# Kernel tuning notes

Measured on AMD Instinct MI355X. Metric: run time of the kernel, lower is better.

Reference implementation:

```python
import jax, jax.numpy as jnp
import numpy as np

N_NODES = 50000
N_EDGES = 1_600_000
DIMS = [512, 256, 128]


def _edge_softmax(vals, rows, n):
    # sparse softmax over dim=1 (per source row), only over stored edges
    m = jax.ops.segment_max(vals, rows, num_segments=n)
    e = jnp.exp(vals - m[rows])
    s = jax.ops.segment_sum(e, rows, num_segments=n)
    return e / s[rows]


def _spmm(att, rows, cols, H, n):
    # (sparse C) @ H : gather source cols, scale by edge weight, scatter-add to rows
    return jax.ops.segment_sum(att[:, None] * H[cols], rows, num_segments=n)


def setup_inputs() -> dict:
    key = jax.random.key(0)
    ks = jax.random.split(key, 12)
    X = jax.random.normal(ks[0], (N_NODES, DIMS[0]), dtype=jnp.float32)
    edge_row = jax.random.randint(ks[1], (N_EDGES,), 0, N_NODES, dtype=jnp.int32)
    edge_col = jax.random.randint(ks[2], (N_EDGES,), 0, N_NODES, dtype=jnp.int32)
    A_vals = jnp.ones((N_EDGES,), dtype=jnp.float32)
    def lin(k, dout, din):
        lim = 1.0 / np.sqrt(din)
        return jax.random.uniform(k, (dout, din), jnp.float32, -lim, lim)
    W0 = lin(ks[3], DIMS[1], DIMS[0])
    b0 = jax.random.uniform(ks[4], (DIMS[1],), jnp.float32, -1/np.sqrt(DIMS[0]), 1/np.sqrt(DIMS[0]))
    W1 = lin(ks[5], DIMS[2], DIMS[1])
    b1 = jax.random.uniform(ks[6], (DIMS[2],), jnp.float32, -1/np.sqrt(DIMS[1]), 1/np.sqrt(DIMS[1]))
    v00 = jax.random.normal(ks[7], (DIMS[1],), dtype=jnp.float32)
    v01 = jax.random.normal(ks[8], (DIMS[1],), dtype=jnp.float32)
    v10 = jax.random.normal(ks[9], (DIMS[2],), dtype=jnp.float32)
    v11 = jax.random.normal(ks[10], (DIMS[2],), dtype=jnp.float32)
    return {"X": X, "edge_row": edge_row, "edge_col": edge_col, "A_vals": A_vals,
            "W0": W0, "b0": b0, "W1": W1, "b1": b1,
            "v00": v00, "v01": v01, "v10": v10, "v11": v11}


def reference(X, edge_row, edge_col, A_vals, W0, b0, W1, b1, v00, v01, v10, v11):
    n = X.shape[0]
    layers = [((W0, b0), (v00, v01)), ((W1, b1), (v10, v11))]
    H = X
    atts = []
    # encoder
    for (W, b), (va, vb) in layers:
        M = H @ W.T + b                               # [N, d_out]
        # attention logits are computed under no_grad in the original
        f1 = M @ va                                   # [N]
        f2 = M @ vb
        logits = jax.lax.stop_gradient(A_vals * (f1[edge_row] + f2[edge_col]))
        att = _edge_softmax(jax.nn.sigmoid(logits), edge_row, n)
        H = _spmm(att, edge_row, edge_col, M, n)
        atts.append(att)
    final_H = H
    # decoder (tied weights, reverse order, reuse encoder attention)
    for ((W, _), _), att in zip(reversed(layers), reversed(atts)):
        H = H @ W                                     # F.linear(H, W.t()) == H @ W
        H = _spmm(att, edge_row, edge_col, H, n)
    return H, final_H
```

## Files before the change

### kernel.cpp

```cpp
#include <hip/hip_runtime.h>
#include <cstdint>
#include <cstddef>

typedef __attribute__((ext_vector_type(8))) short bf16x8;
typedef __attribute__((ext_vector_type(4))) float f32x4;

__device__ __forceinline__ ushort f2b(float f) {
    union { float f; uint32_t u; } v; v.f = f;
    uint32_t r = (v.u + 0x7fffu + ((v.u >> 16) & 1u)) >> 16;
    return (ushort)r;
}
__device__ __forceinline__ float b2f(ushort b) {
    union { uint32_t u; float f; } v; v.u = ((uint32_t)b) << 16;
    return v.f;
}

__device__ __forceinline__ void gll16(const void* g, void* l) {
    __builtin_amdgcn_global_load_lds((const __attribute__((address_space(1))) void*)g,
                                     (__attribute__((address_space(3))) void*)l, 16, 0, 0);
}

__global__ __launch_bounds__(256) void hist_kernel(const int* __restrict__ rows,
                                                   int* __restrict__ bhist, int E, int nb) {
    __shared__ int h[512];
    for (int i = threadIdx.x; i < nb; i += 256) h[i] = 0;
    __syncthreads();
    int stride = gridDim.x * blockDim.x;
    for (int e = blockIdx.x * blockDim.x + threadIdx.x; e < E; e += stride)
        atomicAdd(&h[rows[e] >> 7], 1);
    __syncthreads();
    for (int i = threadIdx.x; i < nb; i += 256)
        if (h[i]) atomicAdd(&bhist[i], h[i]);
}

__global__ __launch_bounds__(512) void scan512(const int* __restrict__ bhist,
                                               int* __restrict__ boff, int* __restrict__ gcur,
                                               int* __restrict__ rp, int nb, int E, int N) {
    __shared__ int sm[512];
    int v = ((int)threadIdx.x < nb) ? bhist[threadIdx.x] : 0;
    sm[threadIdx.x] = v;
    __syncthreads();
    for (int off = 1; off < 512; off <<= 1) {
        int t = ((int)threadIdx.x >= off) ? sm[threadIdx.x - off] : 0;
        __syncthreads();
        sm[threadIdx.x] += t;
        __syncthreads();
    }
    if ((int)threadIdx.x < nb) {
        int e0 = sm[threadIdx.x] - v;
        boff[threadIdx.x] = e0;
        gcur[threadIdx.x] = e0;
    }
    if (threadIdx.x == 0) { boff[nb] = E; rp[N] = E; }
}

__global__ __launch_bounds__(256) void binpass(const int* __restrict__ rows,
                                               const int* __restrict__ cols,
                                               const float* __restrict__ avals,
                                               int* __restrict__ gcur,
                                               uint2* __restrict__ tmp, int E, int nb) {
    __shared__ int hist[512];
    __shared__ int base[512];
    int e0 = blockIdx.x * 4096;
    int nE = min(4096, E - e0);
    for (int i = threadIdx.x; i < nb; i += 256) hist[i] = 0;
    __syncthreads();
    for (int i = threadIdx.x; i < nE; i += 256)
        atomicAdd(&hist[rows[e0 + i] >> 7], 1);
    __syncthreads();
    for (int i = threadIdx.x; i < nb; i += 256) {
        int c = hist[i];
        if (c) base[i] = atomicAdd(&gcur[i], c);
        hist[i] = 0;
    }
    __syncthreads();
    for (int i = threadIdx.x; i < nE; i += 256) {
        int r = rows[e0 + i];
        int b = r >> 7;
        int loc = atomicAdd(&hist[b], 1);
        uint2 t;
        t.x = ((uint32_t)r << 16) | (uint32_t)cols[e0 + i];
        t.y = __float_as_uint(avals[e0 + i]);
        tmp[base[b] + loc] = t;
    }
}

__global__ __launch_bounds__(256) void bucketpass(const uint2* __restrict__ tmp,
                                                  const int* __restrict__ boff,
                                                  int* __restrict__ rp,
                                                  int* __restrict__ col_s,
                                                  float* __restrict__ a_s, int N) {
    __shared__ int cnt[128];
    __shared__ int pre[128];
    int b = blockIdx.x;
    int r0 = b << 7;
    int nr = min(128, N - r0);
    int t0 = boff[b], t1 = boff[b + 1];
    if ((int)threadIdx.x < 128) cnt[threadIdx.x] = 0;
    __syncthreads();
    for (int i = t0 + (int)threadIdx.x; i < t1; i += 256)
        atomicAdd(&cnt[(tmp[i].x >> 16) - r0], 1);
    __syncthreads();
    if ((int)threadIdx.x < 128) pre[threadIdx.x] = cnt[threadIdx.x];
    __syncthreads();
    for (int off = 1; off < 128; off <<= 1) {
        int t = ((int)threadIdx.x >= off && (int)threadIdx.x < 128) ? pre[threadIdx.x - off] : 0;
        __syncthreads();
        if ((int)threadIdx.x < 128) pre[threadIdx.x] += t;
        __syncthreads();
    }
    if ((int)threadIdx.x < nr) {
        int ex = pre[threadIdx.x] - cnt[threadIdx.x];
        rp[r0 + threadIdx.x] = t0 + ex;
        cnt[threadIdx.x] = t0 + ex;
    }
    __syncthreads();
    for (int i = t0 + (int)threadIdx.x; i < t1; i += 256) {
        uint2 t = tmp[i];
        int lr = (int)(t.x >> 16) - r0;
        int pos = atomicAdd(&cnt[lr], 1);
        col_s[pos] = (int)(t.x & 0xffffu);
        a_s[pos] = __uint_as_float(t.y);
    }
}

__global__ __launch_bounds__(256) void wprep(const float* __restrict__ W0,
                                             const float* __restrict__ W1,
                                             const float* __restrict__ b0,
                                             const float* __restrict__ v00,
                                             const float* __restrict__ v01,
                                             float* __restrict__ u0,
                                             float* __restrict__ u1,
                                             float* __restrict__ bp,
                                             float* __restrict__ cc) {
    if (blockIdx.x == 0) {
        int c = threadIdx.x;
        for (int rep = 0; rep < 2; ++rep, c += 256) {
            float s0 = 0.f, s1 = 0.f;
            for (int r = 0; r < 256; ++r) {
                float w = W0[(size_t)r * 512 + c];
                s0 += w * v00[r];
                s1 += w * v01[r];
            }
            u0[c] = s0;
            u1[c] = s1;
        }
    } else {
        int i = threadIdx.x;
        if (i < 128) {
            float s = 0.f;
            for (int k = 0; k < 256; ++k) s += W1[(size_t)i * 256 + k] * b0[k];
            bp[i] = s;
        } else if (i == 128) {
            float s = 0.f;
            for (int k = 0; k < 256; ++k) s += b0[k] * v00[k];
            cc[0] = s;
        } else if (i == 129) {
            float s = 0.f;
            for (int k = 0; k < 256; ++k) s += b0[k] * v01[k];
            cc[1] = s;
        }
    }
}

__global__ __launch_bounds__(256) void convert_fx(const float* __restrict__ X,
                                                  const float* __restrict__ u0,
                                                  const float* __restrict__ u1,
                                                  const float* __restrict__ cc,
                                                  ushort* __restrict__ Xh,
                                                  float* __restrict__ f1,
                                                  float* __restrict__ f2, int N) {
    int w = threadIdx.x >> 6;
    int l = threadIdx.x & 63;
    const float4* U0 = (const float4*)u0;
    const float4* U1 = (const float4*)u1;
    float4 ua = U0[l * 2], ub = U0[l * 2 + 1];
    float4 va = U1[l * 2], vb = U1[l * 2 + 1];
    float c0 = cc[0], c1 = cc[1];
#pragma unroll
    for (int rr = 0; rr < 2; ++rr) {
        int row = blockIdx.x * 8 + w * 2 + rr;
        if (row >= N) return;
        const float4* Xr = (const float4*)(X + (size_t)row * 512);
        float4 x0 = Xr[l * 2], x1 = Xr[l * 2 + 1];
        ushort4 h0, h1;
        h0.x = f2b(x0.x); h0.y = f2b(x0.y); h0.z = f2b(x0.z); h0.w = f2b(x0.w);
        h1.x = f2b(x1.x); h1.y = f2b(x1.y); h1.z = f2b(x1.z); h1.w = f2b(x1.w);
        ushort4* Xo = (ushort4*)(Xh + (size_t)row * 512);
        Xo[l * 2] = h0;
        Xo[l * 2 + 1] = h1;
        float s1 = x0.x * ua.x + x0.y * ua.y + x0.z * ua.z + x0.w * ua.w
                 + x1.x * ub.x + x1.y * ub.y + x1.z * ub.z + x1.w * ub.w;
        float s2 = x0.x * va.x + x0.y * va.y + x0.z * va.z + x0.w * va.w
                 + x1.x * vb.x + x1.y * vb.y + x1.z * vb.z + x1.w * vb.w;
#pragma unroll
        for (int off = 32; off > 0; off >>= 1) {
            s1 += __shfl_xor(s1, off);
            s2 += __shfl_xor(s2, off);
        }
        if (l == 0) { f1[row] = s1 + c0; f2[row] = s2 + c1; }
    }
}

__global__ __launch_bounds__(256) void prep_weights(const float* __restrict__ W0,
                                                    const float* __restrict__ W1,
                                                    ushort* __restrict__ W1h,
                                                    ushort* __restrict__ Wt0h) {
    int i = blockIdx.x * 256 + threadIdx.x;
    float4 v = ((const float4*)W0)[i];
    ushort4 o;
    o.x = f2b(v.x); o.y = f2b(v.y); o.z = f2b(v.z); o.w = f2b(v.w);
    int r = (i * 4) >> 9;
    int c = (i * 4) & 511;
    Wt0h[(size_t)(c + 0) * 256 + r] = o.x;
    Wt0h[(size_t)(c + 1) * 256 + r] = o.y;
    Wt0h[(size_t)(c + 2) * 256 + r] = o.z;
    Wt0h[(size_t)(c + 3) * 256 + r] = o.w;
    if (i < 8192) {
        float4 w = ((const float4*)W1)[i];
        ushort4 p;
        p.x = f2b(w.x); p.y = f2b(w.y); p.z = f2b(w.z); p.w = f2b(w.w);
        ((ushort4*)W1h)[i] = p;
    }
}

__global__ __launch_bounds__(256) void gemm_bf16(const ushort* __restrict__ A,
                                                 const ushort* __restrict__ B,
                                                 const float* __restrict__ bias,
                                                 float* __restrict__ Cf,
                                                 ushort* __restrict__ Ch,
                                                 ushort* __restrict__ ChT,
                                                 int M, int K, int Dout) {
    __shared__ ushort As[128 * 64];
    __shared__ ushort Bs[128 * 64];
    int bm = blockIdx.y * 128, bn = blockIdx.x * 128;
    int tid = threadIdx.x;
    int w = tid >> 6, l = tid & 63;
    int wm = (w & 1) * 64, wn = (w >> 1) * 64;
    int lm = l & 15, quad = l >> 4;
    int wslot = tid & 192;

    f32x4 acc[4][4] = {};

    for (int k0 = 0; k0 < K; k0 += 64) {
#pragma unroll
        for (int it = 0; it < 4; ++it) {
            int slot = it * 256 + tid;
            int row = slot >> 3;
            int qg = ((slot & 7) ^ (row & 7)) * 8;
            int ga = bm + row; if (ga > M - 1) ga = M - 1;
            gll16(A + (size_t)ga * K + k0 + qg, As + (size_t)(it * 256 + wslot) * 8);
            gll16(B + (size_t)(bn + row) * K + k0 + qg, Bs + (size_t)(it * 256 + wslot) * 8);
        }
        __syncthreads();
#pragma unroll
        for (int ks = 0; ks < 2; ++ks) {
            bf16x8 af[4], bfr[4];
#pragma unroll
            for (int i = 0; i < 4; ++i) {
                int r = wm + i * 16 + lm;
                af[i] = *(const bf16x8*)&As[r * 64 + (((ks * 4 + quad) ^ (r & 7)) * 8)];
            }
#pragma unroll
            for (int j = 0; j < 4; ++j) {
                int r = wn + j * 16 + lm;
                bfr[j] = *(const bf16x8*)&Bs[r * 64 + (((ks * 4 + quad) ^ (r & 7)) * 8)];
            }
#pragma unroll
            for (int i = 0; i < 4; ++i)
#pragma unroll
                for (int j = 0; j < 4; ++j)
                    acc[i][j] = __builtin_amdgcn_mfma_f32_16x16x32_bf16(af[i], bfr[j], acc[i][j], 0, 0, 0);
        }
        __syncthreads();
    }

    float bv[4] = {0.f, 0.f, 0.f, 0.f};
    if (bias) {
#pragma unroll
        for (int j = 0; j < 4; ++j) bv[j] = bias[bn + wn + j * 16 + lm];
    }
#pragma unroll
    for (int i = 0; i < 4; ++i) {
#pragma unroll
        for (int r = 0; r < 4; ++r) {
            int row = bm + wm + i * 16 + quad * 4 + r;
            if (row < M) {
#pragma unroll
                for (int j = 0; j < 4; ++j) {
                    int col = bn + wn + j * 16 + lm;
                    float v = acc[i][j][r] + bv[j];
                    if (Cf) Cf[(size_t)row * Dout + col] = v;
                    if (Ch) Ch[(size_t)row * Dout + col] = f2b(v);
                    if (ChT) ChT[(size_t)col * M + row] = f2b(v);
                }
            }
        }
    }
}

__global__ __launch_bounds__(256) void att2_kernel(const int* __restrict__ rp,
                                                   const int* __restrict__ col_s,
                                                   const float* __restrict__ a_s,
                                                   const float* __restrict__ f1,
                                                   const float* __restrict__ f2,
                                                   float* __restrict__ att,
                                                   float* __restrict__ rs, int N) {
    int r = blockIdx.x * 4 + (threadIdx.x >> 6);
    if (r >= N) return;
    int lane = threadIdx.x & 63;
    int beg = rp[r], end = rp[r + 1];
    float fr = f1[r];
    float s = 0.f;
    for (int j = beg + lane; j < end; j += 64) {
        float x = a_s[j] * (fr + f2[col_s[j]]);
        float v = 1.f / (1.f + __expf(-x));
        float e = __expf(v);
        att[j] = e;
        s += e;
    }
#pragma unroll
    for (int off = 32; off > 0; off >>= 1) s += __shfl_xor(s, off);
    if (lane == 0) rs[r] = (end > beg) ? 1.f / s : 0.f;
}

__global__ __launch_bounds__(256) void spmm128(const int* __restrict__ rp,
                                               const int* __restrict__ col_s,
                                               const float* __restrict__ att,
                                               const float* __restrict__ rs,
                                               const ushort* __restrict__ H,
                                               const float* __restrict__ bias,
                                               const float* __restrict__ va,
                                               const float* __restrict__ vb,
                                               float* __restrict__ f1,
                                               float* __restrict__ f2,
                                               ushort* __restrict__ Oh,
                                               float* __restrict__ Of, int N) {
    int r = blockIdx.x * 16 + (threadIdx.x >> 4);
    if (r >= N) return;
    int lane = threadIdx.x & 15;
    int beg = rp[r], end = rp[r + 1];
    float acc[8] = {0.f, 0.f, 0.f, 0.f, 0.f, 0.f, 0.f, 0.f};
    const uint4* H4 = (const uint4*)H;
#define FMA8(h, wgt) { \
        acc[0] += (wgt) * b2f((ushort)((h).x & 0xffffu)); \
        acc[1] += (wgt) * b2f((ushort)((h).x >> 16)); \
        acc[2] += (wgt) * b2f((ushort)((h).y & 0xffffu)); \
        acc[3] += (wgt) * b2f((ushort)((h).y >> 16)); \
        acc[4] += (wgt) * b2f((ushort)((h).z & 0xffffu)); \
        acc[5] += (wgt) * b2f((ushort)((h).z >> 16)); \
        acc[6] += (wgt) * b2f((ushort)((h).w & 0xffffu)); \
        acc[7] += (wgt) * b2f((ushort)((h).w >> 16)); }
    int j = beg;
    for (; j + 4 <= end; j += 4) {
        int c0 = col_s[j], c1 = col_s[j + 1], c2 = col_s[j + 2], c3 = col_s[j + 3];
        float w0 = att[j], w1 = att[j + 1], w2 = att[j + 2], w3 = att[j + 3];
        uint4 h0 = H4[(size_t)c0 * 16 + lane];
        uint4 h1 = H4[(size_t)c1 * 16 + lane];
        uint4 h2 = H4[(size_t)c2 * 16 + lane];
        uint4 h3 = H4[(size_t)c3 * 16 + lane];
        FMA8(h0, w0) FMA8(h1, w1) FMA8(h2, w2) FMA8(h3, w3)
    }
    for (; j < end; ++j) {
        uint4 h = H4[(size_t)col_s[j] * 16 + lane];
        float w0 = att[j];
        FMA8(h, w0)
    }
#undef FMA8
    float rsv = rs[r];
#pragma unroll
    for (int k = 0; k < 8; ++k) acc[k] *= rsv;
    if (bias) {
        const float4* b4 = (const float4*)(bias + lane * 8);
        float4 ba = b4[0], bb = b4[1];
        acc[0] += ba.x; acc[1] += ba.y; acc[2] += ba.z; acc[3] += ba.w;
        acc[4] += bb.x; acc[5] += bb.y; acc[6] += bb.z; acc[7] += bb.w;
    }
    if (va) {
        const float4* a4 = (const float4*)(va + lane * 8);
        const float4* c4 = (const float4*)(vb + lane * 8);
        float4 va0 = a4[0], va1 = a4[1], vb0 = c4[0], vb1 = c4[1];
        float p1 = acc[0] * va0.x + acc[1] * va0.y + acc[2] * va0.z + acc[3] * va0.w
                 + acc[4] * va1.x + acc[5] * va1.y + acc[6] * va1.z + acc[7] * va1.w;
        float p2 = acc[0] * vb0.x + acc[1] * vb0.y + acc[2] * vb0.z + acc[3] * vb0.w
                 + acc[4] * vb1.x + acc[5] * vb1.y + acc[6] * vb1.z + acc[7] * vb1.w;
#pragma unroll
        for (int off = 8; off > 0; off >>= 1) {
            p1 += __shfl_xor(p1, off);
            p2 += __shfl_xor(p2, off);
        }
        if (lane == 0) { f1[r] = p1; f2[r] = p2; }
    }
    if (Oh) {
        uint4 o;
        o.x = (uint32_t)f2b(acc[0]) | ((uint32_t)f2b(acc[1]) << 16);
        o.y = (uint32_t)f2b(acc[2]) | ((uint32_t)f2b(acc[3]) << 16);
        o.z = (uint32_t)f2b(acc[4]) | ((uint32_t)f2b(acc[5]) << 16);
        o.w = (uint32_t)f2b(acc[6]) | ((uint32_t)f2b(acc[7]) << 16);
        ((uint4*)Oh)[(size_t)r * 16 + lane] = o;
    }
    if (Of) {
        float4* O4 = (float4*)Of;
        O4[(size_t)r * 32 + lane * 2]     = make_float4(acc[0], acc[1], acc[2], acc[3]);
        O4[(size_t)r * 32 + lane * 2 + 1] = make_float4(acc[4], acc[5], acc[6], acc[7]);
    }
}

extern "C" void kernel_launch(void* const* d_in, const int* in_sizes, int n_in,
                              void* d_out, int out_size, void* d_ws, size_t ws_size,
                              hipStream_t stream) {
    const float* X    = (const float*)d_in[0];
    const int*   erow = (const int*)d_in[1];
    const int*   ecol = (const int*)d_in[2];
    const float* aval = (const float*)d_in[3];
    const float* W0   = (const float*)d_in[4];
    const float* b0   = (const float*)d_in[5];
    const float* W1   = (const float*)d_in[6];
    const float* b1   = (const float*)d_in[7];
    const float* v00  = (const float*)d_in[8];
    const float* v01  = (const float*)d_in[9];
    const float* v10  = (const float*)d_in[10];
    const float* v11  = (const float*)d_in[11];

    const int D0 = 512, D1 = 256, D2 = 128;
    const int N = in_sizes[0] / D0;
    const int E = in_sizes[1];
    const int NB = (N + 127) / 128;
    float* out = (float*)d_out;

    char* ws = (char*)d_ws;
    size_t off = 0;
    auto alloc = [&](size_t bytes) {
        char* p = ws + off;
        off += (bytes + 255) & ~(size_t)255;
        return p;
    };
    ushort* Xh   = (ushort*)alloc((size_t)N * D0 * 2);
    ushort* Ph   = (ushort*)alloc((size_t)N * D2 * 2);
    ushort* M1h  = (ushort*)alloc((size_t)N * D2 * 2);
    ushort* H2h  = (ushort*)alloc((size_t)N * D2 * 2);
    ushort* S0h  = (ushort*)alloc((size_t)N * D2 * 2);
    ushort* W1h  = (ushort*)alloc((size_t)D2 * D1 * 2);
    ushort* Wt0h = (ushort*)alloc((size_t)D0 * D1 * 2);
    ushort* Wph  = (ushort*)alloc((size_t)D2 * D0 * 2);
    ushort* WfTh = (ushort*)alloc((size_t)D0 * D2 * 2);
    float* att0  = (float*)alloc((size_t)E * 4);
    float* att1  = (float*)alloc((size_t)E * 4);
    float* a_s   = (float*)alloc((size_t)E * 4);
    float* f1    = (float*)alloc((size_t)N * 4);
    float* f2    = (float*)alloc((size_t)N * 4);
    float* rs0   = (float*)alloc((size_t)N * 4);
    float* rs1   = (float*)alloc((size_t)N * 4);
    float* u0    = (float*)alloc(512 * 4);
    float* u1    = (float*)alloc(512 * 4);
    float* bp    = (float*)alloc(128 * 4);
    float* cc    = (float*)alloc(2 * 4);
    int* rp      = (int*)alloc(((size_t)N + 1) * 4);
    int* col_s   = (int*)alloc((size_t)E * 4);
    uint2* tmp   = (uint2*)alloc((size_t)E * 8);
    int* bhist   = (int*)alloc(512 * 4);
    int* boff    = (int*)alloc(513 * 4);
    int* gcur    = (int*)alloc(512 * 4);

    hipMemsetAsync(bhist, 0, 512 * sizeof(int), stream);
    hist_kernel<<<256, 256, 0, stream>>>(erow, bhist, E, NB);
    scan512<<<1, 512, 0, stream>>>(bhist, boff, gcur, rp, NB, E, N);
    binpass<<<(E + 4095) / 4096, 256, 0, stream>>>(erow, ecol, aval, gcur, tmp, E, NB);
    bucketpass<<<NB, 256, 0, stream>>>(tmp, boff, rp, col_s, a_s, N);

    wprep<<<2, 256, 0, stream>>>(W0, W1, b0, v00, v01, u0, u1, bp, cc);
    prep_weights<<<128, 256, 0, stream>>>(W0, W1, W1h, Wt0h);

    convert_fx<<<(N + 7) / 8, 256, 0, stream>>>(X, u0, u1, cc, Xh, f1, f2, N);

    gemm_bf16<<<dim3(4, 1), 256, 0, stream>>>(W1h, Wt0h, nullptr, nullptr, Wph, WfTh,
                                              D2, D1, D0);

    const int gy = (N + 127) / 128;
    const int agrid = (N + 3) / 4;
    const int sgrid = (N + 15) / 16;

    att2_kernel<<<agrid, 256, 0, stream>>>(rp, col_s, a_s, f1, f2, att0, rs0, N);
    gemm_bf16<<<dim3(1, gy), 256, 0, stream>>>(Xh, Wph, bp, nullptr, Ph, nullptr,
                                               N, D0, D2);
    spmm128<<<sgrid, 256, 0, stream>>>(rp, col_s, att0, rs0, Ph, b1, v10, v11, f1, f2,
                                       M1h, nullptr, N);
    att2_kernel<<<agrid, 256, 0, stream>>>(rp, col_s, a_s, f1, f2, att1, rs1, N);
    spmm128<<<sgrid, 256, 0, stream>>>(rp, col_s, att1, rs1, M1h, nullptr,
                                       nullptr, nullptr, nullptr, nullptr,
                                       H2h, out + (size_t)N * D0, N);

    spmm128<<<sgrid, 256, 0, stream>>>(rp, col_s, att1, rs1, H2h, nullptr,
                                       nullptr, nullptr, nullptr, nullptr,
                                       Ph, nullptr, N);
    spmm128<<<sgrid, 256, 0, stream>>>(rp, col_s, att0, rs0, Ph, nullptr,
                                       nullptr, nullptr, nullptr, nullptr,
                                       S0h, nullptr, N);
    gemm_bf16<<<dim3(D0 / 128, gy), 256, 0, stream>>>(S0h, WfTh, nullptr, out, nullptr,
                                                      nullptr, N, D2, D0);
}
```

Baseline: 661.4 us.

## Fuse X bf16 conversion and attention logits into the first GEMM

Replaces the separate convert_fx pass, which wrote a bf16 copy of X and computed f1/f2, with a GEMM that reads fp32 X directly, converts it to bf16 into LDS, and accumulates the f1/f2 dot products along the way. This removes one full write and re-read of the 50000x512 X copy. The weight-prep kernels are merged into one launch with a parallelised u0/u1 reduction, and the SpMM gather loop gains an 8-wide unroll for more loads in flight. In exchange, the GEMM now stages A through registers instead of async global-to-LDS loads, which may expose more latency.

Result: faster. 612.6 us (-7.4%).

```diff
diff --git a/kernel.cpp b/kernel.cpp
--- a/kernel.cpp
+++ b/kernel.cpp
@@ -13,6 +13,12 @@
 __device__ __forceinline__ float b2f(ushort b) {
     union { uint32_t u; float f; } v; v.u = ((uint32_t)b) << 16;
     return v.f;
+}
+__device__ __forceinline__ uint32_t pack2(float a, float b) {
+    return (uint32_t)f2b(a) | ((uint32_t)f2b(b) << 16);
+}
+__device__ __forceinline__ float dot4(float4 a, float4 b) {
+    return a.x * b.x + a.y * b.y + a.z * b.z + a.w * b.w;
 }
 
 __device__ __forceinline__ void gll16(const void* g, void* l) {
@@ -124,29 +130,59 @@
     }
 }
 
-__global__ __launch_bounds__(256) void wprep(const float* __restrict__ W0,
-                                             const float* __restrict__ W1,
-                                             const float* __restrict__ b0,
-                                             const float* __restrict__ v00,
-                                             const float* __restrict__ v01,
-                                             float* __restrict__ u0,
-                                             float* __restrict__ u1,
-                                             float* __restrict__ bp,
-                                             float* __restrict__ cc) {
-    if (blockIdx.x == 0) {
-        int c = threadIdx.x;
-        for (int rep = 0; rep < 2; ++rep, c += 256) {
-            float s0 = 0.f, s1 = 0.f;
-            for (int r = 0; r < 256; ++r) {
-                float w = W0[(size_t)r * 512 + c];
-                s0 += w * v00[r];
-                s1 += w * v01[r];
-            }
-            u0[c] = s0;
-            u1[c] = s1;
+__global__ __launch_bounds__(256) void prep_all(const float* __restrict__ W0,
+                                                const float* __restrict__ W1,
+                                                const float* __restrict__ b0,
+                                                const float* __restrict__ v00,
+                                                const float* __restrict__ v01,
+                                                ushort* __restrict__ W1h,
+                                                ushort* __restrict__ Wt0h,
+                                                float* __restrict__ u0,
+                                                float* __restrict__ u1,
+                                                float* __restrict__ bp,
+                                                float* __restrict__ cc) {
+    __shared__ float su0[256];
+    __shared__ float su1[256];
+    int bid = blockIdx.x;
+    int tid = threadIdx.x;
+    if (bid < 128) {
+        int i = bid * 256 + tid;
+        float4 v = ((const float4*)W0)[i];
+        ushort4 o;
+        o.x = f2b(v.x); o.y = f2b(v.y); o.z = f2b(v.z); o.w = f2b(v.w);
+        int r = (i * 4) >> 9;
+        int c = (i * 4) & 511;
+        Wt0h[(size_t)(c + 0) * 256 + r] = o.x;
+        Wt0h[(size_t)(c + 1) * 256 + r] = o.y;
+        Wt0h[(size_t)(c + 2) * 256 + r] = o.z;
+        Wt0h[(size_t)(c + 3) * 256 + r] = o.w;
+        if (i < 8192) {
+            float4 w = ((const float4*)W1)[i];
+            ushort4 p;
+            p.x = f2b(w.x); p.y = f2b(w.y); p.z = f2b(w.z); p.w = f2b(w.w);
+            ((ushort4*)W1h)[i] = p;
+        }
+    } else if (bid < 144) {
+        int ci = tid & 31;
+        int rl = tid >> 5;
+        int c = (bid - 128) * 32 + ci;
+        float s0 = 0.f, s1 = 0.f;
+        for (int r = rl; r < 256; r += 8) {
+            float w = W0[(size_t)r * 512 + c];
+            s0 += w * v00[r];
+            s1 += w * v01[r];
+        }
+        su0[tid] = s0;
+        su1[tid] = s1;
+        __syncthreads();
+        if (tid < 32) {
+            float a = 0.f, b = 0.f;
+            for (int g = 0; g < 8; ++g) { a += su0[g * 32 + tid]; b += su1[g * 32 + tid]; }
+            u0[c] = a;
+            u1[c] = b;
         }
     } else {
-        int i = threadIdx.x;
+        int i = tid;
         if (i < 128) {
             float s = 0.f;
             for (int k = 0; k < 256; ++k) s += W1[(size_t)i * 256 + k] * b0[k];
@@ -160,67 +196,6 @@
             for (int k = 0; k < 256; ++k) s += b0[k] * v01[k];
             cc[1] = s;
         }
-    }
-}
-
-__global__ __launch_bounds__(256) void convert_fx(const float* __restrict__ X,
-                                                  const float* __restrict__ u0,
-                                                  const float* __restrict__ u1,
-                                                  const float* __restrict__ cc,
-                                                  ushort* __restrict__ Xh,
-                                                  float* __restrict__ f1,
-                                                  float* __restrict__ f2, int N) {
-    int w = threadIdx.x >> 6;
-    int l = threadIdx.x & 63;
-    const float4* U0 = (const float4*)u0;
-    const float4* U1 = (const float4*)u1;
-    float4 ua = U0[l * 2], ub = U0[l * 2 + 1];
-    float4 va = U1[l * 2], vb = U1[l * 2 + 1];
-    float c0 = cc[0], c1 = cc[1];
-#pragma unroll
-    for (int rr = 0; rr < 2; ++rr) {
-        int row = blockIdx.x * 8 + w * 2 + rr;
-        if (row >= N) return;
-        const float4* Xr = (const float4*)(X + (size_t)row * 512);
-        float4 x0 = Xr[l * 2], x1 = Xr[l * 2 + 1];
-        ushort4 h0, h1;
-        h0.x = f2b(x0.x); h0.y = f2b(x0.y); h0.z = f2b(x0.z); h0.w = f2b(x0.w);
-        h1.x = f2b(x1.x); h1.y = f2b(x1.y); h1.z = f2b(x1.z); h1.w = f2b(x1.w);
-        ushort4* Xo = (ushort4*)(Xh + (size_t)row * 512);
-        Xo[l * 2] = h0;
-        Xo[l * 2 + 1] = h1;
-        float s1 = x0.x * ua.x + x0.y * ua.y + x0.z * ua.z + x0.w * ua.w
-                 + x1.x * ub.x + x1.y * ub.y + x1.z * ub.z + x1.w * ub.w;
-        float s2 = x0.x * va.x + x0.y * va.y + x0.z * va.z + x0.w * va.w
-                 + x1.x * vb.x + x1.y * vb.y + x1.z * vb.z + x1.w * vb.w;
-#pragma unroll
-        for (int off = 32; off > 0; off >>= 1) {
-            s1 += __shfl_xor(s1, off);
-            s2 += __shfl_xor(s2, off);
-        }
-        if (l == 0) { f1[row] = s1 + c0; f2[row] = s2 + c1; }
-    }
-}
-
-__global__ __launch_bounds__(256) void prep_weights(const float* __restrict__ W0,
-                                                    const float* __restrict__ W1,
-                                                    ushort* __restrict__ W1h,
-                                                    ushort* __restrict__ Wt0h) {
-    int i = blockIdx.x * 256 + threadIdx.x;
-    float4 v = ((const float4*)W0)[i];
-    ushort4 o;
-    o.x = f2b(v.x); o.y = f2b(v.y); o.z = f2b(v.z); o.w = f2b(v.w);
-    int r = (i * 4) >> 9;
-    int c = (i * 4) & 511;
-    Wt0h[(size_t)(c + 0) * 256 + r] = o.x;
-    Wt0h[(size_t)(c + 1) * 256 + r] = o.y;
-    Wt0h[(size_t)(c + 2) * 256 + r] = o.z;
-    Wt0h[(size_t)(c + 3) * 256 + r] = o.w;
-    if (i < 8192) {
-        float4 w = ((const float4*)W1)[i];
-        ushort4 p;
-        p.x = f2b(w.x); p.y = f2b(w.y); p.z = f2b(w.z); p.w = f2b(w.w);
-        ((ushort4*)W1h)[i] = p;
     }
 }
 
@@ -293,6 +268,115 @@
                     if (Cf) Cf[(size_t)row * Dout + col] = v;
                     if (Ch) Ch[(size_t)row * Dout + col] = f2b(v);
                     if (ChT) ChT[(size_t)col * M + row] = f2b(v);
+                }
+            }
+        }
+    }
+}
+
+__global__ __launch_bounds__(256) void gemm_xp(const float* __restrict__ X,
+                                               const ushort* __restrict__ B,
+                                               const float* __restrict__ bp,
+                                               const float* __restrict__ u0,
+                                               const float* __restrict__ u1,
+                                               const float* __restrict__ cc,
+                                               ushort* __restrict__ Ph,
+                                               float* __restrict__ f1,
+                                               float* __restrict__ f2,
+                                               int M, int K) {
+    __shared__ ushort As[128 * 64];
+    __shared__ ushort Bs[128 * 64];
+    int bm = blockIdx.y * 128;
+    int tid = threadIdx.x;
+    int w = tid >> 6, l = tid & 63;
+    int wm = (w & 1) * 64, wn = (w >> 1) * 64;
+    int lm = l & 15, quad = l >> 4;
+    int wslot = tid & 192;
+    int ar = tid >> 2;
+    int aq = tid & 3;
+
+    f32x4 acc[4][4] = {};
+    float fA1 = 0.f, fA2 = 0.f, fB1 = 0.f, fB2 = 0.f;
+
+    for (int k0 = 0; k0 < K; k0 += 64) {
+#pragma unroll
+        for (int it = 0; it < 4; ++it) {
+            int slot = it * 256 + tid;
+            int row = slot >> 3;
+            int qg = ((slot & 7) ^ (row & 7)) * 8;
+            gll16(B + (size_t)row * K + k0 + qg, Bs + (size_t)(it * 256 + wslot) * 8);
+        }
+        const float4* U0 = (const float4*)(u0 + k0 + aq * 16);
+        const float4* U1 = (const float4*)(u1 + k0 + aq * 16);
+        float4 ua0 = U0[0], ua1 = U0[1], ua2 = U0[2], ua3 = U0[3];
+        float4 va0 = U1[0], va1 = U1[1], va2 = U1[2], va3 = U1[3];
+#pragma unroll
+        for (int rr = 0; rr < 2; ++rr) {
+            int row = ar + rr * 64;
+            int ga = bm + row; if (ga > M - 1) ga = M - 1;
+            const float4* src = (const float4*)(X + (size_t)ga * K + k0 + aq * 16);
+            float4 x0 = src[0], x1 = src[1], x2 = src[2], x3 = src[3];
+            float s1 = dot4(x0, ua0) + dot4(x1, ua1) + dot4(x2, ua2) + dot4(x3, ua3);
+            float s2 = dot4(x0, va0) + dot4(x1, va1) + dot4(x2, va2) + dot4(x3, va3);
+            if (rr == 0) { fA1 += s1; fA2 += s2; } else { fB1 += s1; fB2 += s2; }
+            uint4 pa, pb;
+            pa.x = pack2(x0.x, x0.y); pa.y = pack2(x0.z, x0.w);
+            pa.z = pack2(x1.x, x1.y); pa.w = pack2(x1.z, x1.w);
+            pb.x = pack2(x2.x, x2.y); pb.y = pack2(x2.z, x2.w);
+            pb.z = pack2(x3.x, x3.y); pb.w = pack2(x3.z, x3.w);
+            int c0 = (aq * 2) ^ (row & 7);
+            int c1 = (aq * 2 + 1) ^ (row & 7);
+            *(uint4*)&As[row * 64 + c0 * 8] = pa;
+            *(uint4*)&As[row * 64 + c1 * 8] = pb;
+        }
+        __syncthreads();
+#pragma unroll
+        for (int ks = 0; ks < 2; ++ks) {
+            bf16x8 af[4], bfr[4];
+#pragma unroll
+            for (int i = 0; i < 4; ++i) {
+                int r = wm + i * 16 + lm;
+                af[i] = *(const bf16x8*)&As[r * 64 + (((ks * 4 + quad) ^ (r & 7)) * 8)];
+            }
+#pragma unroll
+            for (int j = 0; j < 4; ++j) {
+                int r = wn + j * 16 + lm;
+                bfr[j] = *(const bf16x8*)&Bs[r * 64 + (((ks * 4 + quad) ^ (r & 7)) * 8)];
+            }
+#pragma unroll
+            for (int i = 0; i < 4; ++i)
+#pragma unroll
+                for (int j = 0; j < 4; ++j)
+                    acc[i][j] = __builtin_amdgcn_mfma_f32_16x16x32_bf16(af[i], bfr[j], acc[i][j], 0, 0, 0);
+        }
+        __syncthreads();
+    }
+
+    fA1 += __shfl_xor(fA1, 1); fA1 += __shfl_xor(fA1, 2);
+    fA2 += __shfl_xor(fA2, 1); fA2 += __shfl_xor(fA2, 2);
+    fB1 += __shfl_xor(fB1, 1); fB1 += __shfl_xor(fB1, 2);
+    fB2 += __shfl_xor(fB2, 1); fB2 += __shfl_xor(fB2, 2);
+    if (aq == 0) {
+        float c0 = cc[0], c1 = cc[1];
+        int r0 = bm + ar;
+        if (r0 < M) { f1[r0] = fA1 + c0; f2[r0] = fA2 + c1; }
+        int r1 = r0 + 64;
+        if (r1 < M) { f1[r1] = fB1 + c0; f2[r1] = fB2 + c1; }
+    }
+
+    float bv[4];
+#pragma unroll
+    for (int j = 0; j < 4; ++j) bv[j] = bp[wn + j * 16 + lm];
+#pragma unroll
+    for (int i = 0; i < 4; ++i) {
+#pragma unroll
+        for (int r = 0; r < 4; ++r) {
+            int row = bm + wm + i * 16 + quad * 4 + r;
+            if (row < M) {
+#pragma unroll
+                for (int j = 0; j < 4; ++j) {
+                    int col = wn + j * 16 + lm;
+                    Ph[(size_t)row * 128 + col] = f2b(acc[i][j][r] + bv[j]);
                 }
             }
         }
@@ -352,6 +436,22 @@
         acc[6] += (wgt) * b2f((ushort)((h).w & 0xffffu)); \
         acc[7] += (wgt) * b2f((ushort)((h).w >> 16)); }
     int j = beg;
+    for (; j + 8 <= end; j += 8) {
+        int c0 = col_s[j],     c1 = col_s[j + 1], c2 = col_s[j + 2], c3 = col_s[j + 3];
+        int c4 = col_s[j + 4], c5 = col_s[j + 5], c6 = col_s[j + 6], c7 = col_s[j + 7];
+        float w0 = att[j],     w1 = att[j + 1], w2 = att[j + 2], w3 = att[j + 3];
+        float w4 = att[j + 4], w5 = att[j + 5], w6 = att[j + 6], w7 = att[j + 7];
+        uint4 h0 = H4[(size_t)c0 * 16 + lane];
+        uint4 h1 = H4[(size_t)c1 * 16 + lane];
+        uint4 h2 = H4[(size_t)c2 * 16 + lane];
+        uint4 h3 = H4[(size_t)c3 * 16 + lane];
+        uint4 h4 = H4[(size_t)c4 * 16 + lane];
+        uint4 h5 = H4[(size_t)c5 * 16 + lane];
+        uint4 h6 = H4[(size_t)c6 * 16 + lane];
+        uint4 h7 = H4[(size_t)c7 * 16 + lane];
+        FMA8(h0, w0) FMA8(h1, w1) FMA8(h2, w2) FMA8(h3, w3)
+        FMA8(h4, w4) FMA8(h5, w5) FMA8(h6, w6) FMA8(h7, w7)
+    }
     for (; j + 4 <= end; j += 4) {
         int c0 = col_s[j], c1 = col_s[j + 1], c2 = col_s[j + 2], c3 = col_s[j + 3];
         float w0 = att[j], w1 = att[j + 1], w2 = att[j + 2], w3 = att[j + 3];
@@ -435,7 +535,6 @@
         off += (bytes + 255) & ~(size_t)255;
         return p;
     };
-    ushort* Xh   = (ushort*)alloc((size_t)N * D0 * 2);
     ushort* Ph   = (ushort*)alloc((size_t)N * D2 * 2);
     ushort* M1h  = (ushort*)alloc((size_t)N * D2 * 2);
     ushort* H2h  = (ushort*)alloc((size_t)N * D2 * 2);
@@ -468,10 +567,7 @@
     binpass<<<(E + 4095) / 4096, 256, 0, stream>>>(erow, ecol, aval, gcur, tmp, E, NB);
     bucketpass<<<NB, 256, 0, stream>>>(tmp, boff, rp, col_s, a_s, N);
 
-    wprep<<<2, 256, 0, stream>>>(W0, W1, b0, v00, v01, u0, u1, bp, cc);
-    prep_weights<<<128, 256, 0, stream>>>(W0, W1, W1h, Wt0h);
-
-    convert_fx<<<(N + 7) / 8, 256, 0, stream>>>(X, u0, u1, cc, Xh, f1, f2, N);
+    prep_all<<<145, 256, 0, stream>>>(W0, W1, b0, v00, v01, W1h, Wt0h, u0, u1, bp, cc);
 
     gemm_bf16<<<dim3(4, 1), 256, 0, stream>>>(W1h, Wt0h, nullptr, nullptr, Wph, WfTh,
                                               D2, D1, D0);
@@ -480,9 +576,8 @@
     const int agrid = (N + 3) / 4;
     const int sgrid = (N + 15) / 16;
 
+    gemm_xp<<<dim3(1, gy), 256, 0, stream>>>(X, Wph, bp, u0, u1, cc, Ph, f1, f2, N, D0);
     att2_kernel<<<agrid, 256, 0, stream>>>(rp, col_s, a_s, f1, f2, att0, rs0, N);
-    gemm_bf16<<<dim3(1, gy), 256, 0, stream>>>(Xh, Wph, bp, nullptr, Ph, nullptr,
-                                               N, D0, D2);
     spmm128<<<sgrid, 256, 0, stream>>>(rp, col_s, att0, rs0, Ph, b1, v10, v11, f1, f2,
                                        M1h, nullptr, N);
     att2_kernel<<<agrid, 256, 0, stream>>>(rp, col_s, a_s, f1, f2, att1, rs1, N);
```
